# Kernel optimization log

Measured on AMD Instinct MI355X. Metric: run time of the kernel, lower is better.

The kernel has to match this reference:

```python
import jax, jax.numpy as jnp
import numpy as np

B, C, H, W = 4, 256, 224, 224
WH = WW = 8
SH = SW = 4
HEADS = 8
HD = C // HEADS
N = WH * WW
EPS = 1e-5


def _rel_index():
    coords = np.stack(np.meshgrid(np.arange(WH), np.arange(WW), indexing='ij')).reshape(2, -1)
    rel = (coords[:, :, None] - coords[:, None, :]).transpose(1, 2, 0).copy()
    rel[:, :, 0] += WH - 1
    rel[:, :, 1] += WW - 1
    rel[:, :, 0] *= 2 * WW - 1
    return rel.sum(-1)  # (N, N) int

REL_INDEX = _rel_index()


def _shift_mask(Hp, Wp):
    # Swin shift mask for one image: (nW, N, N) float, 0 or -100
    img = np.zeros((Hp, Wp))
    cnt = 0
    for a, b in [(0, Hp - WH), (Hp - WH, Hp - SH), (Hp - SH, Hp)]:
        for c, d in [(0, Wp - WW), (Wp - WW, Wp - SW), (Wp - SW, Wp)]:
            img[a:b, c:d] = cnt
            cnt += 1
    mw = img.reshape(Hp // WH, WH, Wp // WW, WW).transpose(0, 2, 1, 3).reshape(-1, N)
    diff = mw[:, None, :] - mw[:, :, None]  # [w, i, j] = mw[w,j] - mw[w,i]
    return np.where(diff != 0, np.float32(-100.0), np.float32(0.0)).astype(np.float32)


def _ln(x, w, b):
    m = jnp.mean(x, axis=-1, keepdims=True)
    v = jnp.mean(jnp.square(x - m), axis=-1, keepdims=True)
    return (x - m) * jax.lax.rsqrt(v + EPS) * w + b


def setup_inputs() -> dict:
    key = jax.random.key(0)
    ks = jax.random.split(key, 8)
    num_rel = (2 * WH - 1) * (2 * WW - 1)
    return {
        'x': jax.random.normal(ks[0], (B, C, H, W), dtype=jnp.float32),
        'qkv_w': jax.random.normal(ks[1], (3 * C, C), dtype=jnp.float32) * 0.02,
        'proj_w': jax.random.normal(ks[2], (C, C), dtype=jnp.float32) * 0.02,
        'proj_b': jnp.zeros((C,), dtype=jnp.float32),
        'rpb_table': jax.random.normal(ks[3], (num_rel, HEADS), dtype=jnp.float32) * 0.02,
        'norm1_w': jnp.ones((C,), dtype=jnp.float32),
        'norm1_b': jnp.zeros((C,), dtype=jnp.float32),
        'norm2_w': jnp.ones((C,), dtype=jnp.float32),
        'norm2_b': jnp.zeros((C,), dtype=jnp.float32),
        'mlp_w1': jax.random.normal(ks[4], (4 * C, C), dtype=jnp.float32) * 0.02,
        'mlp_b1': jnp.zeros((4 * C,), dtype=jnp.float32),
        'mlp_w2': jax.random.normal(ks[5], (C, 4 * C), dtype=jnp.float32) * 0.02,
        'mlp_b2': jnp.zeros((C,), dtype=jnp.float32),
    }


def reference(x, qkv_w, proj_w, proj_b, rpb_table, norm1_w, norm1_b,
              norm2_w, norm2_b, mlp_w1, mlp_b1, mlp_w2, mlp_b2):
    Bx, Cx, Hx, Wx = x.shape
    pad_h = (WH - Hx % WH) % WH
    pad_w = (WW - Wx % WW) % WW
    if pad_h or pad_w:
        x = jnp.pad(x, ((0, 0), (0, 0), (0, pad_h), (0, pad_w)))
    Hp, Wp = Hx + pad_h, Wx + pad_w
    x = jnp.transpose(x, (0, 2, 3, 1))                    # BHWC
    x = jnp.roll(x, (-SH, -SW), axis=(1, 2))
    nW = (Hp // WH) * (Wp // WW)
    # window partition -> (B*nW, N, C), batch-major
    xw = x.reshape(Bx, Hp // WH, WH, Wp // WW, WW, Cx)
    xw = jnp.transpose(xw, (0, 1, 3, 2, 4, 5)).reshape(-1, N, Cx)

    # ----- windowed attention -----
    h = _ln(xw, norm1_w, norm1_b)
    qkv = (h @ qkv_w.T).reshape(-1, N, 3, HEADS, HD)
    qkv = jnp.transpose(qkv, (2, 0, 3, 1, 4))             # (3, Bw, heads, N, hd)
    q, k, v = qkv[0], qkv[1], qkv[2]
    attn = jnp.einsum('bhnd,bhmd->bhnm', q, k) * (1.0 / HD ** 0.5)
    bias = jnp.transpose(rpb_table[REL_INDEX.reshape(-1)].reshape(N, N, HEADS), (2, 0, 1))
    attn = attn + bias[None]
    # faithful to torch: repeat_interleave(B, dim=0) -> window-major mask ordering
    mask = jnp.asarray(_shift_mask(Hp, Wp))               # (nW, N, N)
    attn = attn + jnp.repeat(mask, Bx, axis=0)[:, None]
    attn = jax.nn.softmax(attn, axis=-1)
    out = jnp.einsum('bhnm,bhmd->bhnd', attn, v)
    out = jnp.transpose(out, (0, 2, 1, 3)).reshape(-1, N, Cx)
    out = out @ proj_w.T + proj_b
    xw = xw + out

    # ----- MLP -----
    h = _ln(xw, norm2_w, norm2_b)
    h = jax.nn.gelu(h @ mlp_w1.T + mlp_b1, approximate=False) @ mlp_w2.T + mlp_b2
    xw = xw + h

    # window reverse, un-shift, un-pad
    x = xw.reshape(Bx, Hp // WH, Wp // WW, WH, WW, Cx)
    x = jnp.transpose(x, (0, 1, 3, 2, 4, 5)).reshape(Bx, Hp, Wp, Cx)
    x = jnp.roll(x, (SH, SW), axis=(1, 2))
    x = x[:, :Hx, :Wx, :]
    return jnp.transpose(x, (0, 3, 1, 2))
```

## Files before the change

### kernel.cpp

```cpp
#include <hip/hip_runtime.h>

typedef unsigned short u16;
typedef unsigned int   u32;
typedef __attribute__((ext_vector_type(8))) __bf16 bf16x8;
typedef __attribute__((ext_vector_type(4))) float  f32x4;
typedef __attribute__((ext_vector_type(4))) u16    u16x4;

#define DEV __device__ __forceinline__

DEV u16 f2b(float f) {
  union { float f; u32 u; } a; a.f = f;
  const u32 u = a.u;
  return (u16)((u + 0x7fffu + ((u >> 16) & 1u)) >> 16);
}

DEV float gelu_fast(float x) {
  const float x2 = x * x;
  const float t  = __builtin_fmaf(0.1029430f, x2, 2.3022150f);
  const float e  = __builtin_exp2f(x * t);
  const float r  = __builtin_amdgcn_rcpf(1.0f + e);
  return __builtin_fmaf(-x, r, x);
}

DEV void gload16(const void* g, void* l) {
  __builtin_amdgcn_global_load_lds(
      (const __attribute__((address_space(1))) void*)g,
      (__attribute__((address_space(3))) void*)l, 16, 0, 0);
}

__global__ __launch_bounds__(256)
void conv_weights(const float* __restrict__ qkvw, const float* __restrict__ projw,
                  const float* __restrict__ w1,   const float* __restrict__ w2,
                  u16* __restrict__ dq, u16* __restrict__ dp,
                  u16* __restrict__ d1, u16* __restrict__ d2) {
  const int t = blockIdx.x * 256 + threadIdx.x;
  if (t < 196608)      dq[t]          = f2b(qkvw[t]);
  else if (t < 262144) dp[t - 196608] = f2b(projw[t - 196608]);
  else if (t < 524288) d1[t - 262144] = f2b(w1[t - 262144]);
  else                 d2[t - 524288] = f2b(w2[t - 524288]);
}

__global__ __launch_bounds__(256)
void ln1_win(const float* __restrict__ x, const float* __restrict__ w1,
             const float* __restrict__ b1, u16* __restrict__ hout,
             float* __restrict__ xwout) {
  __shared__ float xt[64 * 257];
  __shared__ float smean[256], srstd[256];
  const int tid = threadIdx.x, lane = tid & 63, wv = tid >> 6;
  const int g = blockIdx.x;
  const int b = g / 196, rem = g % 196;
  const int wh = rem / 7, wg = rem % 7;
  const int base_r = b * 784 + wh * 28 + wg * 4;
  const int pr = tid >> 5, pc = tid & 31;
  int hp = wh * 8 + 4 + pr; if (hp >= 224) hp -= 224;
  int wp = wg * 32 + 4 + pc; if (wp >= 224) wp -= 224;
  const long roff = (long)b * 256 * 50176 + hp * 224 + wp;

  float s = 0.f, q = 0.f;
  for (int cc = 0; cc < 4; ++cc) {
#pragma unroll 8
    for (int i = 0; i < 64; ++i) {
      const int c = cc * 64 + i;
      const float v = x[(long)c * 50176 + roff];
      xt[i * 257 + tid] = v;
      s += v; q += v * v;
    }
    __syncthreads();
#pragma unroll 8
    for (int jj = 0; jj < 64; ++jj) {
      const int p = jj * 4 + wv;
      const int m = (base_r + ((p & 31) >> 3)) * 64 + (p >> 5) * 8 + (p & 7);
      xwout[(long)m * 256 + cc * 64 + lane] = xt[lane * 257 + p];
    }
    __syncthreads();
  }
  const float mean = s * (1.f / 256.f);
  smean[tid] = mean;
  srstd[tid] = rsqrtf(q * (1.f / 256.f) - mean * mean + 1e-5f);
  __syncthreads();

  float wr_[4], br_[4];
#pragma unroll
  for (int cc = 0; cc < 4; ++cc) { wr_[cc] = w1[cc * 64 + lane]; br_[cc] = b1[cc * 64 + lane]; }
#pragma unroll 2
  for (int jj = 0; jj < 64; ++jj) {
    const int p = jj * 4 + wv;
    const int m = (base_r + ((p & 31) >> 3)) * 64 + (p >> 5) * 8 + (p & 7);
    const float mu = smean[p], rs = srstd[p];
#pragma unroll
    for (int cc = 0; cc < 4; ++cc) {
      const float v = xwout[(long)m * 256 + cc * 64 + lane];
      hout[(long)m * 256 + cc * 64 + lane] = f2b((v - mu) * rs * wr_[cc] + br_[cc]);
    }
  }
}

template<int EPI, int NCOL>
__global__ __launch_bounds__(512, 4)
void gemm_bt(const u16* __restrict__ A, const u16* __restrict__ Bw, const int K,
             float* __restrict__ fout, const float* __restrict__ bias,
             u16* __restrict__ bout,
             const float* __restrict__ lnw, const float* __restrict__ lnb) {
  __shared__ __align__(16) u16 smem[24576];
  u16* sA0 = smem;
  u16* sB0 = smem + 4096;
  u16* sA1 = smem + 12288;
  u16* sB1 = smem + 16384;

  const int tid  = threadIdx.x;
  const int lane = tid & 63;
  const int wid  = tid >> 6;
  const int wrr  = wid >> 2;
  const int wcc  = wid & 3;

  const int nwg = gridDim.x;
  const int bid = blockIdx.x;
  const int wg  = (bid & 7) * (nwg >> 3) + (bid >> 3);
  const int row0 = wg * 128;

  const f32x4 vzero = {0.f, 0.f, 0.f, 0.f};

  const int l15  = lane & 15;
  const int l4   = lane >> 4;
  const int ksw2 = (l15 >> 1) & 3;
  const int lcol = (((tid & 3) ^ ((tid >> 3) & 3)) << 3);

  const u16* pA = A + (long)(row0 + (tid >> 2)) * K + lcol;
  const int wbase = wid * 512;

#define STAGE_TILE(KT, DA, DB)                  \
  {                                             \
    gload16(pA  + (KT), (DA) + wbase);          \
    gload16(pB  + (KT), (DB) + wbase);          \
    gload16(pB2 + (KT), (DB) + 4096 + wbase);   \
  }

#define COMPUTE_TILE(SA, SB, SWAP)                                                      \
  {                                                                                     \
    bf16x8 af[4], bfv[4];                                                               \
    _Pragma("unroll")                                                                   \
    for (int mi = 0; mi < 4; ++mi)                                                      \
      af[mi] = *(const bf16x8*)((SA) + (wrr * 64 + mi * 16 + l15) * 32 +                \
                                ((l4 ^ ksw2) << 3));                                    \
    _Pragma("unroll")                                                                   \
    for (int nj = 0; nj < 4; ++nj)                                                      \
      bfv[nj] = *(const bf16x8*)((SB) + (wcc * 64 + nj * 16 + l15) * 32 +               \
                                 ((l4 ^ ksw2) << 3));                                   \
    _Pragma("unroll")                                                                   \
    for (int mi = 0; mi < 4; ++mi)                                                      \
      _Pragma("unroll")                                                                 \
      for (int nj = 0; nj < 4; ++nj) {                                                  \
        if (SWAP)                                                                       \
          acc[mi][nj] = __builtin_amdgcn_mfma_f32_16x16x32_bf16(bfv[nj], af[mi],        \
                                                                acc[mi][nj], 0, 0, 0);  \
        else                                                                            \
          acc[mi][nj] = __builtin_amdgcn_mfma_f32_16x16x32_bf16(af[mi], bfv[nj],        \
                                                                acc[mi][nj], 0, 0, 0);  \
      }                                                                                 \
  }

#define KLOOP(SWAP)                                                  \
  {                                                                  \
    const int nt = K >> 5;                                           \
    STAGE_TILE(0, sA0, sB0);                                         \
    int cur = 0;                                                     \
    for (int t = 0; t < nt; ++t) {                                   \
      u16* cA = cur ? sA1 : sA0;                                     \
      u16* cB = cur ? sB1 : sB0;                                     \
      u16* nA = cur ? sA0 : sA1;                                     \
      u16* nB = cur ? sB0 : sB1;                                     \
      if (t + 1 < nt) {                                              \
        STAGE_TILE((t + 1) << 5, nA, nB);                            \
        asm volatile("s_waitcnt vmcnt(3)" ::: "memory");             \
      } else {                                                       \
        asm volatile("s_waitcnt vmcnt(0)" ::: "memory");             \
      }                                                              \
      __builtin_amdgcn_s_barrier();                                  \
      asm volatile("" ::: "memory");                                 \
      COMPUTE_TILE(cA, cB, SWAP);                                    \
      asm volatile("" ::: "memory");                                 \
      __builtin_amdgcn_s_barrier();                                  \
      cur ^= 1;                                                      \
    }                                                                \
  }

#pragma unroll
  for (int cb = 0; cb < NCOL; ++cb) {
    const int col0 = cb * 256;
    const u16* pB  = Bw + (long)(col0 + (tid >> 2)) * K + lcol;
    const u16* pB2 = pB + (long)128 * K;

    f32x4 acc[4][4];
#pragma unroll
    for (int i = 0; i < 4; ++i)
#pragma unroll
      for (int j = 0; j < 4; ++j) acc[i][j] = vzero;

    if (EPI == 0 && cb == 2) {
      KLOOP(0);
#pragma unroll
      for (int mi = 0; mi < 4; ++mi) {
        const int mb = row0 + wrr * 64 + mi * 16 + (l4 << 2);
        const int rrg = mb >> 6, ii = mb & 63;
#pragma unroll
        for (int nj = 0; nj < 4; ++nj) {
          const int n = 512 + wcc * 64 + nj * 16 + l15;
          const int hh = (n >> 5) & 7, d = n & 31;
          u16x4 p;
#pragma unroll
          for (int reg = 0; reg < 4; ++reg) p[reg] = f2b(acc[mi][nj][reg]);
          *(u16x4*)(bout + 102760448L + (long)((rrg * 8 + hh) * 32 + d) * 64 + ii) = p;
        }
      }
      continue;
    }

    KLOOP(1);

    if (EPI == 0) {
#pragma unroll
      for (int mi = 0; mi < 4; ++mi) {
        const int m = row0 + wrr * 64 + mi * 16 + l15;
        const int rr = m >> 6, ii = m & 63;
#pragma unroll
        for (int nj = 0; nj < 4; ++nj) {
          const int n = col0 + wcc * 64 + nj * 16 + (l4 << 2);
          const int s = n >> 8, hh = (n >> 5) & 7, d = n & 31;
          u16x4 p;
#pragma unroll
          for (int reg = 0; reg < 4; ++reg) p[reg] = f2b(acc[mi][nj][reg]);
          *(u16x4*)(bout + (long)s * 51380224L +
                    (long)((rr * 8 + hh) * 64 + ii) * 32 + d) = p;
        }
      }
    } else if (EPI == 1) {
      f32x4 b4[4];
#pragma unroll
      for (int nj = 0; nj < 4; ++nj)
        b4[nj] = *(const f32x4*)(bias + wcc * 64 + nj * 16 + (l4 << 2));
      float sS[4], sQ[4];
#pragma unroll
      for (int mi = 0; mi < 4; ++mi) {
        const int m = row0 + wrr * 64 + mi * 16 + l15;
        float* yrow = fout + (long)m * 256;
        float s = 0.f, q = 0.f;
#pragma unroll
        for (int nj = 0; nj < 4; ++nj) {
          const int n = wcc * 64 + nj * 16 + (l4 << 2);
          f32x4 o = *(f32x4*)(yrow + n);
#pragma unroll
          for (int reg = 0; reg < 4; ++reg) {
            o[reg] += acc[mi][nj][reg] + b4[nj][reg];
            s += o[reg]; q += o[reg] * o[reg];
          }
          *(f32x4*)(yrow + n) = o;
          acc[mi][nj] = o;
        }
        s += __shfl_xor(s, 16); s += __shfl_xor(s, 32);
        q += __shfl_xor(q, 16); q += __shfl_xor(q, 32);
        sS[mi] = s; sQ[mi] = q;
      }
      float* ps = (float*)smem;
      float* pq = ps + 512;
      __syncthreads();
      if (lane < 16) {
#pragma unroll
        for (int mi = 0; mi < 4; ++mi) {
          const int idx = (wrr * 64 + mi * 16 + l15) * 4 + wcc;
          ps[idx] = sS[mi]; pq[idx] = sQ[mi];
        }
      }
      __syncthreads();
#pragma unroll
      for (int mi = 0; mi < 4; ++mi) {
        const int m = row0 + wrr * 64 + mi * 16 + l15;
        const int base = (wrr * 64 + mi * 16 + l15) * 4;
        const float S = ps[base] + ps[base + 1] + ps[base + 2] + ps[base + 3];
        const float Q = pq[base] + pq[base + 1] + pq[base + 2] + pq[base + 3];
        const float mean = S * (1.f / 256.f);
        const float rstd = rsqrtf(Q * (1.f / 256.f) - mean * mean + 1e-5f);
#pragma unroll
        for (int nj = 0; nj < 4; ++nj) {
          const int n = wcc * 64 + nj * 16 + (l4 << 2);
          const f32x4 w4 = *(const f32x4*)(lnw + n);
          const f32x4 c4 = *(const f32x4*)(lnb + n);
          u16x4 p;
#pragma unroll
          for (int reg = 0; reg < 4; ++reg)
            p[reg] = f2b((acc[mi][nj][reg] - mean) * rstd * w4[reg] + c4[reg]);
          *(u16x4*)(bout + (long)m * 256 + n) = p;
        }
      }
    }
  }
#undef STAGE_TILE
#undef COMPUTE_TILE
#undef KLOOP
}

__global__ __launch_bounds__(512, 2)
void mlp_fused(const u16* __restrict__ A, const u16* __restrict__ w1b,
               const u16* __restrict__ w2b, const float* __restrict__ y,
               const float* __restrict__ b1, const float* __restrict__ b2,
               float* __restrict__ oout) {
  __shared__ __align__(16) u16 smem[57344];
  u16* sA0 = smem;
  u16* sB0 = smem + 4096;
  u16* sA1 = smem + 12288;
  u16* sB1 = smem + 16384;
  u16* H   = smem + 24576;

  const int tid  = threadIdx.x;
  const int lane = tid & 63;
  const int wid  = tid >> 6;
  const int wrr  = wid >> 2;
  const int wcc  = wid & 3;

  const int nwg = gridDim.x;
  const int bid = blockIdx.x;
  const int wg  = (bid & 7) * (nwg >> 3) + (bid >> 3);
  const int row0 = wg * 128;

  const f32x4 vzero = {0.f, 0.f, 0.f, 0.f};
  const int l15  = lane & 15;
  const int l4   = lane >> 4;
  const int ksw2 = (l15 >> 1) & 3;
  const int lcol = (((tid & 3) ^ ((tid >> 3) & 3)) << 3);

  const u16* pA = A + (long)(row0 + (tid >> 2)) * 256 + lcol;
  const int wbase = wid * 512;

  f32x4 acc2[4][4];
#pragma unroll
  for (int i = 0; i < 4; ++i)
#pragma unroll
    for (int j = 0; j < 4; ++j) acc2[i][j] = vzero;

#define RD_FRAG(BUF, R0, OFF) \
  (*(const bf16x8*)((BUF) + ((R0) + l15) * 32 + ((l4 ^ ksw2) << 3) + (OFF)))

  for (int cb = 0; cb < 4; ++cb) {
    const u16* pB  = w1b + (long)(cb * 256 + (tid >> 2)) * 256 + lcol;
    const u16* pB2 = pB + 128 * 256;

    f32x4 acc[4][4];
#pragma unroll
    for (int i = 0; i < 4; ++i)
#pragma unroll
      for (int j = 0; j < 4; ++j) acc[i][j] = vzero;

    {
      gload16(pA, sA0 + wbase);
      gload16(pB, sB0 + wbase);
      gload16(pB2, sB0 + 4096 + wbase);
      int cur = 0;
      for (int t = 0; t < 8; ++t) {
        u16* cA = cur ? sA1 : sA0;
        u16* cB = cur ? sB1 : sB0;
        u16* nA = cur ? sA0 : sA1;
        u16* nB = cur ? sB0 : sB1;
        if (t + 1 < 8) {
          const int kt = (t + 1) << 5;
          gload16(pA + kt, nA + wbase);
          gload16(pB + kt, nB + wbase);
          gload16(pB2 + kt, nB + 4096 + wbase);
          asm volatile("s_waitcnt vmcnt(3)" ::: "memory");
        } else {
          asm volatile("s_waitcnt vmcnt(0)" ::: "memory");
        }
        __builtin_amdgcn_s_barrier();
        asm volatile("" ::: "memory");
        {
          bf16x8 af[4], bfv[4];
#pragma unroll
          for (int mi = 0; mi < 4; ++mi) af[mi] = RD_FRAG(cA, wrr * 64 + mi * 16, 0);
#pragma unroll
          for (int nj = 0; nj < 4; ++nj) bfv[nj] = RD_FRAG(cB, wcc * 64 + nj * 16, 0);
#pragma unroll
          for (int mi = 0; mi < 4; ++mi)
#pragma unroll
            for (int nj = 0; nj < 4; ++nj)
              acc[mi][nj] = __builtin_amdgcn_mfma_f32_16x16x32_bf16(
                  bfv[nj], af[mi], acc[mi][nj], 0, 0, 0);
        }
        asm volatile("" ::: "memory");
        __builtin_amdgcn_s_barrier();
        cur ^= 1;
      }
    }

    {
      f32x4 b4[4];
#pragma unroll
      for (int nj = 0; nj < 4; ++nj)
        b4[nj] = *(const f32x4*)(b1 + cb * 256 + wcc * 64 + nj * 16 + (l4 << 2));
#pragma unroll
      for (int mi = 0; mi < 4; ++mi) {
        const int m = wrr * 64 + mi * 16 + l15;
#pragma unroll
        for (int nj = 0; nj < 4; ++nj) {
          u16x4 p;
#pragma unroll
          for (int reg = 0; reg < 4; ++reg)
            p[reg] = f2b(gelu_fast(acc[mi][nj][reg] + b4[nj][reg]));
          const int kt   = wcc * 2 + (nj >> 1);
          const int slot = ((nj & 1) << 1) + (l4 >> 1);
          *(u16x4*)(H + kt * 4096 + m * 32 +
                    ((slot ^ ((m >> 1) & 3)) << 3) + ((l4 & 1) << 2)) = p;
        }
      }
    }
    __syncthreads();

    {
      const u16* qB  = w2b + (long)(tid >> 2) * 1024 + cb * 256 + lcol;
      const u16* qB2 = qB + 128 * 1024;
      gload16(qB, sB0 + wbase);
      gload16(qB2, sB0 + 4096 + wbase);
      int cur = 0;
      for (int kt = 0; kt < 8; ++kt) {
        u16* cB = cur ? sB1 : sB0;
        u16* nB = cur ? sB0 : sB1;
        if (kt + 1 < 8) {
          const int ko = (kt + 1) << 5;
          gload16(qB + ko, nB + wbase);
          gload16(qB2 + ko, nB + 4096 + wbase);
          asm volatile("s_waitcnt vmcnt(2)" ::: "memory");
        } else {
          asm volatile("s_waitcnt vmcnt(0)" ::: "memory");
        }
        __builtin_amdgcn_s_barrier();
        asm volatile("" ::: "memory");
        {
          const u16* Hk = H + kt * 4096;
          bf16x8 af[4], bfv[4];
#pragma unroll
          for (int mi = 0; mi < 4; ++mi) af[mi] = RD_FRAG(Hk, wrr * 64 + mi * 16, 0);
#pragma unroll
          for (int nj = 0; nj < 4; ++nj) bfv[nj] = RD_FRAG(cB, wcc * 64 + nj * 16, 0);
#pragma unroll
          for (int mi = 0; mi < 4; ++mi)
#pragma unroll
            for (int nj = 0; nj < 4; ++nj)
              acc2[mi][nj] = __builtin_amdgcn_mfma_f32_16x16x32_bf16(
                  bfv[nj], af[mi], acc2[mi][nj], 0, 0, 0);
        }
        asm volatile("" ::: "memory");
        __builtin_amdgcn_s_barrier();
        cur ^= 1;
      }
    }
    __syncthreads();
  }
#undef RD_FRAG

  {
    f32x4 b4[4];
#pragma unroll
    for (int nj = 0; nj < 4; ++nj)
      b4[nj] = *(const f32x4*)(b2 + wcc * 64 + nj * 16 + (l4 << 2));
#pragma unroll
    for (int mi = 0; mi < 4; ++mi) {
      const int m = row0 + wrr * 64 + mi * 16 + l15;
      const float* yrow = y + (long)m * 256;
#pragma unroll
      for (int nj = 0; nj < 4; ++nj) {
        const int n = wcc * 64 + nj * 16 + (l4 << 2);
        const f32x4 yv = *(const f32x4*)(yrow + n);
#pragma unroll
        for (int reg = 0; reg < 4; ++reg)
          acc2[mi][nj][reg] += yv[reg] + b4[nj][reg];
      }
    }
    const int wr0 = row0 >> 6;
    const int b = wr0 / 784, rem = wr0 % 784;
    const int wh = rem / 28, wwb = rem % 28;
    float* tp = (float*)smem;
    const int pidx = tid & 127, cgrp = tid >> 7;
    const int pr = pidx >> 4, pc = pidx & 15;
    int hp = wh * 8 + 4 + pr;  if (hp >= 224) hp -= 224;
    int wp = wwb * 8 + 4 + pc; if (wp >= 224) wp -= 224;
    float* ob = oout + (long)b * 256 * 50176 + hp * 224 + wp;
#pragma unroll
    for (int cc = 0; cc < 4; ++cc) {
      __syncthreads();
      if (wcc == cc) {
#pragma unroll
        for (int mi = 0; mi < 4; ++mi) {
          const int ml = wrr * 64 + mi * 16 + l15;
          const int px = ((ml & 63) >> 3) * 16 + (ml >> 6) * 8 + (ml & 7);
#pragma unroll
          for (int nj = 0; nj < 4; ++nj)
#pragma unroll
            for (int reg = 0; reg < 4; ++reg)
              tp[(nj * 16 + (l4 << 2) + reg) * 128 + (px ^ (l4 << 2))] =
                  acc2[mi][nj][reg];
        }
      }
      __syncthreads();
#pragma unroll 4
      for (int j = 0; j < 16; ++j) {
        const int cl = cgrp * 16 + j;
        ob[(long)(cc * 64 + cl) * 50176] =
            tp[cl * 128 + (pidx ^ (((cl >> 2) & 3) << 2))];
      }
    }
  }
}

__global__ __launch_bounds__(256)
void attn_win(const u16* __restrict__ qkv, const float* __restrict__ rpb,
              u16* __restrict__ aout) {
  __shared__ u16 Pl[4][4096];
  __shared__ float srpb[1800];
  const int tid = threadIdx.x, lane = tid & 63, wv = tid >> 6;
  const int bid = blockIdx.x;
  const int r = bid >> 1;
  const int h = (bid & 1) * 4 + wv;
  for (int i = tid; i < 1800; i += 256) srpb[i] = rpb[i];
  __syncthreads();

  const int midx = r >> 2;
  const int wh = midx / 28, ww = midx % 28;
  const int l15 = lane & 15, l4 = lane >> 4;

  u16* Pw = &Pl[wv][0];
  const long hb = (long)(r * 8 + h) * 2048;
  const u16* qh = qkv + hb;
  const u16* kh = qkv + 51380224 + hb;
  const u16* vh = qkv + 102760448 + hb;

  int rj[4], cj[4], labj[4];
#pragma unroll
  for (int nj = 0; nj < 4; ++nj) {
    const int j = nj * 16 + l15;
    rj[nj] = j >> 3; cj[nj] = j & 7;
    const int hp = wh * 8 + rj[nj], wp = ww * 8 + cj[nj];
    const int lh = (hp < 216) ? 0 : ((hp < 220) ? 1 : 2);
    const int lw = (wp < 216) ? 0 : ((wp < 220) ? 1 : 2);
    labj[nj] = lh * 3 + lw;
  }

  const f32x4 vzero = {0.f, 0.f, 0.f, 0.f};

  bf16x8 qf[4], kf[4];
#pragma unroll
  for (int mi = 0; mi < 4; ++mi)
    qf[mi] = *(const bf16x8*)(qh + (mi * 16 + l15) * 32 + l4 * 8);
#pragma unroll
  for (int nj = 0; nj < 4; ++nj)
    kf[nj] = *(const bf16x8*)(kh + (nj * 16 + l15) * 32 + l4 * 8);

  f32x4 S[4][4];
#pragma unroll
  for (int mi = 0; mi < 4; ++mi)
#pragma unroll
    for (int nj = 0; nj < 4; ++nj)
      S[mi][nj] = __builtin_amdgcn_mfma_f32_16x16x32_bf16(qf[mi], kf[nj], vzero, 0, 0, 0);

#pragma unroll
  for (int mi = 0; mi < 4; ++mi)
#pragma unroll
    for (int reg = 0; reg < 4; ++reg) {
      const int i = mi * 16 + (l4 << 2) + reg;
      const int ri = i >> 3, ci = i & 7;
      const int hp = wh * 8 + ri, wp = ww * 8 + ci;
      const int lh = (hp < 216) ? 0 : ((hp < 220) ? 1 : 2);
      const int lw = (wp < 216) ? 0 : ((wp < 220) ? 1 : 2);
      const int li = lh * 3 + lw;
      float v[4];
#pragma unroll
      for (int nj = 0; nj < 4; ++nj) {
        const int idx = (ri - rj[nj] + 7) * 15 + (ci - cj[nj] + 7);
        v[nj] = S[mi][nj][reg] * 0.17677669529663687f + srpb[idx * 8 + h]
              + ((li != labj[nj]) ? -100.0f : 0.0f);
      }
      float mx = fmaxf(fmaxf(v[0], v[1]), fmaxf(v[2], v[3]));
      mx = fmaxf(mx, __shfl_xor(mx, 1));
      mx = fmaxf(mx, __shfl_xor(mx, 2));
      mx = fmaxf(mx, __shfl_xor(mx, 4));
      mx = fmaxf(mx, __shfl_xor(mx, 8));
      float sum = 0.f;
#pragma unroll
      for (int nj = 0; nj < 4; ++nj) { v[nj] = __expf(v[nj] - mx); sum += v[nj]; }
      sum += __shfl_xor(sum, 1);
      sum += __shfl_xor(sum, 2);
      sum += __shfl_xor(sum, 4);
      sum += __shfl_xor(sum, 8);
      const float rinv = __builtin_amdgcn_rcpf(sum);
      const int sw = (i & 7) << 3;
#pragma unroll
      for (int nj = 0; nj < 4; ++nj)
        Pw[i * 64 + ((nj * 16 + l15) ^ sw)] = f2b(v[nj] * rinv);
    }

  f32x4 OT[2][4];
#pragma unroll
  for (int td = 0; td < 2; ++td)
#pragma unroll
    for (int ti = 0; ti < 4; ++ti) OT[td][ti] = vzero;

  const int rsw = (l15 & 7) << 3;
#pragma unroll
  for (int kk = 0; kk < 2; ++kk) {
    bf16x8 pf[4], vf[2];
#pragma unroll
    for (int ti = 0; ti < 4; ++ti)
      pf[ti] = *(const bf16x8*)(Pw + (ti * 16 + l15) * 64 + ((kk * 32 + l4 * 8) ^ rsw));
#pragma unroll
    for (int td = 0; td < 2; ++td)
      vf[td] = *(const bf16x8*)(vh + (td * 16 + l15) * 64 + kk * 32 + l4 * 8);
#pragma unroll
    for (int td = 0; td < 2; ++td)
#pragma unroll
      for (int ti = 0; ti < 4; ++ti)
        OT[td][ti] = __builtin_amdgcn_mfma_f32_16x16x32_bf16(vf[td], pf[ti], OT[td][ti], 0, 0, 0);
  }

#pragma unroll
  for (int td = 0; td < 2; ++td)
#pragma unroll
    for (int ti = 0; ti < 4; ++ti) {
      const int i = ti * 16 + l15;
      const int d0 = td * 16 + (l4 << 2);
      u16x4 p;
#pragma unroll
      for (int reg = 0; reg < 4; ++reg) p[reg] = f2b(OT[td][ti][reg]);
      *(u16x4*)(aout + (long)(r * 64 + i) * 256 + h * 32 + d0) = p;
    }
}

extern "C" void kernel_launch(void* const* d_in, const int* in_sizes, int n_in,
                              void* d_out, int out_size, void* d_ws, size_t ws_size,
                              hipStream_t stream) {
  (void)in_sizes; (void)n_in; (void)out_size; (void)ws_size;
  const float* x     = (const float*)d_in[0];
  const float* qkvw  = (const float*)d_in[1];
  const float* projw = (const float*)d_in[2];
  const float* projb = (const float*)d_in[3];
  const float* rpb   = (const float*)d_in[4];
  const float* n1w   = (const float*)d_in[5];
  const float* n1b   = (const float*)d_in[6];
  const float* n2w   = (const float*)d_in[7];
  const float* n2b   = (const float*)d_in[8];
  const float* w1    = (const float*)d_in[9];
  const float* b1    = (const float*)d_in[10];
  const float* w2    = (const float*)d_in[11];
  const float* b2    = (const float*)d_in[12];

  char* ws = (char*)d_ws;
  u16*   hbuf   = (u16*)(ws);
  u16*   qkvb   = (u16*)(ws + 102760448);
  u16*   abuf   = (u16*)(ws + 411041792);
  float* ybuf   = (float*)(ws + 513802240);
  u16*   qkvwb  = (u16*)(ws + 719323136);
  u16*   projwb = (u16*)(ws + 719716352);
  u16*   w1b    = (u16*)(ws + 719847424);
  u16*   w2b    = (u16*)(ws + 720371712);

  conv_weights<<<3072, 256, 0, stream>>>(qkvw, projw, w1, w2, qkvwb, projwb, w1b, w2b);
  ln1_win<<<784, 256, 0, stream>>>(x, n1w, n1b, hbuf, ybuf);
  gemm_bt<0, 3><<<1568, 512, 0, stream>>>(hbuf, qkvwb, 256, nullptr, nullptr, qkvb, nullptr, nullptr);
  attn_win<<<6272, 256, 0, stream>>>(qkvb, rpb, abuf);
  gemm_bt<1, 1><<<1568, 512, 0, stream>>>(abuf, projwb, 256, ybuf, projb, hbuf, n2w, n2b);
  mlp_fused<<<1568, 512, 0, stream>>>(hbuf, w1b, w2b, ybuf, b1, b2, (float*)d_out);
}
```

Baseline: 1.063 ms.

## Shrink MLP hidden chunk to 128 to halve LDS and raise occupancy

The fused MLP kernel now processes the 1024-wide hidden dimension in eight chunks of 128 instead of four chunks of 256. This halves the first-GEMM accumulator tiles, unifies the A/B double buffers, and cuts LDS from 112KB to 64KB. Launch bounds go from 2 to 4 blocks per CU to allow more resident workgroups for latency hiding. In exchange there are twice as many chunk iterations with extra barriers, the A tile is reloaded more often, and register pressure rises under the tighter launch bound, which may cause spills.

After: 1.162 ms. +9.3%, slower.

```diff
diff --git a/kernel.cpp b/kernel.cpp
--- a/kernel.cpp
+++ b/kernel.cpp
@@ -298,17 +298,15 @@
 #undef KLOOP
 }
 
-__global__ __launch_bounds__(512, 2)
+__global__ __launch_bounds__(512, 4)
 void mlp_fused(const u16* __restrict__ A, const u16* __restrict__ w1b,
                const u16* __restrict__ w2b, const float* __restrict__ y,
                const float* __restrict__ b1, const float* __restrict__ b2,
                float* __restrict__ oout) {
-  __shared__ __align__(16) u16 smem[57344];
-  u16* sA0 = smem;
-  u16* sB0 = smem + 4096;
-  u16* sA1 = smem + 12288;
-  u16* sB1 = smem + 16384;
-  u16* H   = smem + 24576;
+  __shared__ __align__(16) u16 smem[32768];
+  u16* buf0 = smem;
+  u16* buf1 = smem + 8192;
+  u16* H    = smem + 16384;
 
   const int tid  = threadIdx.x;
   const int lane = tid & 63;
@@ -336,123 +334,117 @@
 #pragma unroll
     for (int j = 0; j < 4; ++j) acc2[i][j] = vzero;
 
-#define RD_FRAG(BUF, R0, OFF) \
-  (*(const bf16x8*)((BUF) + ((R0) + l15) * 32 + ((l4 ^ ksw2) << 3) + (OFF)))
-
-  for (int cb = 0; cb < 4; ++cb) {
-    const u16* pB  = w1b + (long)(cb * 256 + (tid >> 2)) * 256 + lcol;
-    const u16* pB2 = pB + 128 * 256;
-
-    f32x4 acc[4][4];
+  for (int cc = 0; cc < 8; ++cc) {
+    const u16* pB = w1b + (long)(cc * 128 + (tid >> 2)) * 256 + lcol;
+
+    f32x4 acc[4][2];
 #pragma unroll
     for (int i = 0; i < 4; ++i)
 #pragma unroll
-      for (int j = 0; j < 4; ++j) acc[i][j] = vzero;
+      for (int j = 0; j < 2; ++j) acc[i][j] = vzero;
+
+    gload16(pA, buf0 + wbase);
+    gload16(pB, buf0 + 4096 + wbase);
+    int cur = 0;
+    for (int t = 0; t < 8; ++t) {
+      u16* cbuf = cur ? buf1 : buf0;
+      u16* nbuf = cur ? buf0 : buf1;
+      if (t + 1 < 8) {
+        const int kt = (t + 1) << 5;
+        gload16(pA + kt, nbuf + wbase);
+        gload16(pB + kt, nbuf + 4096 + wbase);
+        asm volatile("s_waitcnt vmcnt(2)" ::: "memory");
+      } else {
+        asm volatile("s_waitcnt vmcnt(0)" ::: "memory");
+      }
+      __builtin_amdgcn_s_barrier();
+      asm volatile("" ::: "memory");
+      {
+        bf16x8 af[4], bfv[2];
+#pragma unroll
+        for (int mi = 0; mi < 4; ++mi)
+          af[mi] = *(const bf16x8*)(cbuf + (wrr * 64 + mi * 16 + l15) * 32 +
+                                    ((l4 ^ ksw2) << 3));
+#pragma unroll
+        for (int nj = 0; nj < 2; ++nj)
+          bfv[nj] = *(const bf16x8*)(cbuf + 4096 + (wcc * 32 + nj * 16 + l15) * 32 +
+                                     ((l4 ^ ksw2) << 3));
+#pragma unroll
+        for (int mi = 0; mi < 4; ++mi)
+#pragma unroll
+          for (int nj = 0; nj < 2; ++nj)
+            acc[mi][nj] = __builtin_amdgcn_mfma_f32_16x16x32_bf16(
+                bfv[nj], af[mi], acc[mi][nj], 0, 0, 0);
+      }
+      asm volatile("" ::: "memory");
+      __builtin_amdgcn_s_barrier();
+      cur ^= 1;
+    }
+
+    const u16* qB  = w2b + (long)(tid >> 2) * 1024 + cc * 128 + lcol;
+    const u16* qB2 = qB + 128 * 1024;
+    gload16(qB, buf0 + wbase);
+    gload16(qB2, buf0 + 4096 + wbase);
 
     {
-      gload16(pA, sA0 + wbase);
-      gload16(pB, sB0 + wbase);
-      gload16(pB2, sB0 + 4096 + wbase);
-      int cur = 0;
-      for (int t = 0; t < 8; ++t) {
-        u16* cA = cur ? sA1 : sA0;
-        u16* cB = cur ? sB1 : sB0;
-        u16* nA = cur ? sA0 : sA1;
-        u16* nB = cur ? sB0 : sB1;
-        if (t + 1 < 8) {
-          const int kt = (t + 1) << 5;
-          gload16(pA + kt, nA + wbase);
-          gload16(pB + kt, nB + wbase);
-          gload16(pB2 + kt, nB + 4096 + wbase);
-          asm volatile("s_waitcnt vmcnt(3)" ::: "memory");
-        } else {
-          asm volatile("s_waitcnt vmcnt(0)" ::: "memory");
-        }
-        __builtin_amdgcn_s_barrier();
-        asm volatile("" ::: "memory");
-        {
-          bf16x8 af[4], bfv[4];
-#pragma unroll
-          for (int mi = 0; mi < 4; ++mi) af[mi] = RD_FRAG(cA, wrr * 64 + mi * 16, 0);
-#pragma unroll
-          for (int nj = 0; nj < 4; ++nj) bfv[nj] = RD_FRAG(cB, wcc * 64 + nj * 16, 0);
-#pragma unroll
-          for (int mi = 0; mi < 4; ++mi)
-#pragma unroll
-            for (int nj = 0; nj < 4; ++nj)
-              acc[mi][nj] = __builtin_amdgcn_mfma_f32_16x16x32_bf16(
-                  bfv[nj], af[mi], acc[mi][nj], 0, 0, 0);
-        }
-        asm volatile("" ::: "memory");
-        __builtin_amdgcn_s_barrier();
-        cur ^= 1;
-      }
-    }
-
-    {
-      f32x4 b4[4];
-#pragma unroll
-      for (int nj = 0; nj < 4; ++nj)
-        b4[nj] = *(const f32x4*)(b1 + cb * 256 + wcc * 64 + nj * 16 + (l4 << 2));
+      f32x4 b4[2];
+#pragma unroll
+      for (int nj = 0; nj < 2; ++nj)
+        b4[nj] = *(const f32x4*)(b1 + cc * 128 + wcc * 32 + nj * 16 + (l4 << 2));
 #pragma unroll
       for (int mi = 0; mi < 4; ++mi) {
         const int m = wrr * 64 + mi * 16 + l15;
 #pragma unroll
-        for (int nj = 0; nj < 4; ++nj) {
+        for (int nj = 0; nj < 2; ++nj) {
           u16x4 p;
 #pragma unroll
           for (int reg = 0; reg < 4; ++reg)
             p[reg] = f2b(gelu_fast(acc[mi][nj][reg] + b4[nj][reg]));
-          const int kt   = wcc * 2 + (nj >> 1);
-          const int slot = ((nj & 1) << 1) + (l4 >> 1);
-          *(u16x4*)(H + kt * 4096 + m * 32 +
+          const int slot = nj * 2 + (l4 >> 1);
+          *(u16x4*)(H + wcc * 4096 + m * 32 +
                     ((slot ^ ((m >> 1) & 3)) << 3) + ((l4 & 1) << 2)) = p;
         }
       }
     }
     __syncthreads();
 
-    {
-      const u16* qB  = w2b + (long)(tid >> 2) * 1024 + cb * 256 + lcol;
-      const u16* qB2 = qB + 128 * 1024;
-      gload16(qB, sB0 + wbase);
-      gload16(qB2, sB0 + 4096 + wbase);
-      int cur = 0;
-      for (int kt = 0; kt < 8; ++kt) {
-        u16* cB = cur ? sB1 : sB0;
-        u16* nB = cur ? sB0 : sB1;
-        if (kt + 1 < 8) {
-          const int ko = (kt + 1) << 5;
-          gload16(qB + ko, nB + wbase);
-          gload16(qB2 + ko, nB + 4096 + wbase);
-          asm volatile("s_waitcnt vmcnt(2)" ::: "memory");
-        } else {
-          asm volatile("s_waitcnt vmcnt(0)" ::: "memory");
-        }
-        __builtin_amdgcn_s_barrier();
-        asm volatile("" ::: "memory");
-        {
-          const u16* Hk = H + kt * 4096;
-          bf16x8 af[4], bfv[4];
-#pragma unroll
-          for (int mi = 0; mi < 4; ++mi) af[mi] = RD_FRAG(Hk, wrr * 64 + mi * 16, 0);
-#pragma unroll
-          for (int nj = 0; nj < 4; ++nj) bfv[nj] = RD_FRAG(cB, wcc * 64 + nj * 16, 0);
-#pragma unroll
-          for (int mi = 0; mi < 4; ++mi)
-#pragma unroll
-            for (int nj = 0; nj < 4; ++nj)
-              acc2[mi][nj] = __builtin_amdgcn_mfma_f32_16x16x32_bf16(
-                  bfv[nj], af[mi], acc2[mi][nj], 0, 0, 0);
-        }
-        asm volatile("" ::: "memory");
-        __builtin_amdgcn_s_barrier();
-        cur ^= 1;
-      }
-    }
-    __syncthreads();
-  }
-#undef RD_FRAG
+    cur = 0;
+    for (int kt = 0; kt < 4; ++kt) {
+      u16* cbuf = cur ? buf1 : buf0;
+      u16* nbuf = cur ? buf0 : buf1;
+      if (kt + 1 < 4) {
+        const int ko = (kt + 1) << 5;
+        gload16(qB + ko, nbuf + wbase);
+        gload16(qB2 + ko, nbuf + 4096 + wbase);
+        asm volatile("s_waitcnt vmcnt(2)" ::: "memory");
+      } else {
+        asm volatile("s_waitcnt vmcnt(0)" ::: "memory");
+      }
+      __builtin_amdgcn_s_barrier();
+      asm volatile("" ::: "memory");
+      {
+        const u16* Hk = H + kt * 4096;
+        bf16x8 af[4], bfv[4];
+#pragma unroll
+        for (int mi = 0; mi < 4; ++mi)
+          af[mi] = *(const bf16x8*)(Hk + (wrr * 64 + mi * 16 + l15) * 32 +
+                                    ((l4 ^ ksw2) << 3));
+#pragma unroll
+        for (int nj = 0; nj < 4; ++nj)
+          bfv[nj] = *(const bf16x8*)(cbuf + (wcc * 64 + nj * 16 + l15) * 32 +
+                                     ((l4 ^ ksw2) << 3));
+#pragma unroll
+        for (int mi = 0; mi < 4; ++mi)
+#pragma unroll
+          for (int nj = 0; nj < 4; ++nj)
+            acc2[mi][nj] = __builtin_amdgcn_mfma_f32_16x16x32_bf16(
+                bfv[nj], af[mi], acc2[mi][nj], 0, 0, 0);
+      }
+      asm volatile("" ::: "memory");
+      __builtin_amdgcn_s_barrier();
+      cur ^= 1;
+    }
+  }
 
   {
     f32x4 b4[4];
```
